# Optimization experiments

Measured on AMD Instinct MI355X. Metric: run time of the kernel, lower is better.

The kernel has to match this reference:

```python
import jax, jax.numpy as jnp
import numpy as np

T, B, D, H = 110, 256, 512, 512
EPS = 1e-9


def _forward(a, v, l, qmask, umask, mu_a, mu_v, mu_l, shifta, shiftv,
             turna, turnb, W1, b1, W2, b2):
    Tcur = a.shape[0]
    # ca = mu * (cos(a) + i sin(a)) = mu * exp(i a)
    ca = mu_a[:Tcur] * jnp.exp(1j * a)          # (T,B,D) complex64
    cv = mu_v[:Tcur] * jnp.exp(1j * v)
    cl = mu_l[:Tcur] * jnp.exp(1j * l)
    # phase shift of a and v streams, then sum into lav
    features = cl + ca * jnp.exp(1j * shifta) + cv * jnp.exp(1j * shiftv)  # (T,B,D)

    # --- step 0 (special-cased in the original loop) ---
    temp0 = features[0]                          # (B,D) complex
    qa0 = qmask[0][:, 0:1]                       # (B,1)
    qb0 = qmask[0][:, 1:2]
    ones = jnp.ones_like(temp0) * (1.0 + 1.0j)   # pA=pB=1+1j initial state
    pA0 = (1.0 - qa0) * ones + qa0 * temp0
    pB0 = (1.0 - qb0) * ones + qb0 * temp0

    # --- steps 1..T-1 as a fused scan over time ---
    def step(carry, xs):
        pA, pB = carry
        f, qm, ta, tb = xs                       # f:(B,D) cplx, qm:(B,2), ta/tb:(1,D)
        qa = qm[:, 0:1]
        qb = qm[:, 1:2]
        turn = qa * (pA * jnp.exp(1j * ta)) + qb * (pB * jnp.exp(1j * tb))
        # torch: turn.where(turn==0, turn/(abs+eps)) -> keep 0 where 0, else normalize
        turn = jnp.where(turn == 0, turn, turn / (jnp.abs(turn) + EPS))
        temp = f + turn
        pA = (1.0 - qa) * pA + qa * temp
        pB = (1.0 - qb) * pB + qb * temp
        return (pA, pB), temp

    (_, _), temps = jax.lax.scan(
        step, (pA0, pB0),
        (features[1:], qmask[1:], turna[1:Tcur], turnb[1:Tcur]))

    feats = jnp.concatenate([temp0[None], temps], axis=0)  # (T,B,D) complex
    fr, fi = feats.real, feats.imag
    f1r = fr @ W1.T + b1
    f1i = fi @ W1.T + b1
    f2r = fr @ W2.T + b2
    f2i = fi @ W2.T + b2
    xr = f1r - f2i
    xi = f1i + f2r
    return xr + xi                               # (T,B,H) float32


def setup_inputs() -> dict:
    key = jax.random.key(0)
    ks = jax.random.split(key, 12)
    a = jax.random.normal(ks[0], (T, B, D), jnp.float32)
    v = jax.random.normal(ks[1], (T, B, D), jnp.float32)
    l = jax.random.normal(ks[2], (T, B, D), jnp.float32)
    spk = jax.random.randint(ks[3], (T, B), 0, 2)
    qmask = jax.nn.one_hot(spk, 2, dtype=jnp.float32)      # (T,B,2)
    umask = jnp.ones((T, B), jnp.float32)                  # unused by forward
    mu_a = jnp.ones((110, 1, 1), jnp.float32)
    mu_v = jnp.ones((110, 1, 1), jnp.float32)
    mu_l = jnp.ones((110, 1, 1), jnp.float32)
    shifta = jax.random.normal(ks[4], (1, 1, D), jnp.float32)
    shiftv = jax.random.normal(ks[5], (1, 1, D), jnp.float32)
    turna = jax.random.uniform(ks[6], (110, 1, D), jnp.float32)
    turnb = jax.random.uniform(ks[7], (110, 1, D), jnp.float32)
    W1 = jax.random.normal(ks[8], (H, D), jnp.float32) * 0.02
    b1 = jnp.zeros((H,), jnp.float32)
    W2 = jax.random.normal(ks[9], (H, D), jnp.float32) * 0.02
    b2 = jnp.zeros((H,), jnp.float32)
    return {"a": a, "v": v, "l": l, "qmask": qmask, "umask": umask,
            "mu_a": mu_a, "mu_v": mu_v, "mu_l": mu_l,
            "shifta": shifta, "shiftv": shiftv,
            "turna": turna, "turnb": turnb,
            "W1": W1, "b1": b1, "W2": W2, "b2": b2,
            "dia_len": T}


def reference(a, v, l, qmask, umask, mu_a, mu_v, mu_l, shifta, shiftv,
              turna, turnb, W1, b1, W2, b2, dia_len):
    return _forward(a, v, l, qmask, umask, mu_a, mu_v, mu_l,
                    shifta, shiftv, turna, turnb, W1, b1, W2, b2)
```

## Files before the change

### kernel.cpp

```cpp
#include <hip/hip_runtime.h>

#define T_DIM 110
#define B_DIM 256
#define D_DIM 512
#define H_DIM 512
#define K_CAT 1024
#define M_DIM (T_DIM * B_DIM)
#define BD    (B_DIM * D_DIM)
#define EPSV 1e-9f

typedef float f32x4 __attribute__((ext_vector_type(4)));
typedef short bf16x8 __attribute__((ext_vector_type(8)));

static __device__ __forceinline__ unsigned short f2bf(float f) {
    unsigned u = __builtin_bit_cast(unsigned, f);
    u += 0x7fffu + ((u >> 16) & 1u);
    return (unsigned short)(u >> 16);
}

__global__ __launch_bounds__(256) void prep_w_kernel(
    const float* __restrict__ W1, const float* __restrict__ b1,
    const float* __restrict__ W2,
    unsigned short* __restrict__ Bt,
    float* __restrict__ bias2)
{
    int i = blockIdx.x * 256 + threadIdx.x;
    if (i < H_DIM) bias2[i] = 2.0f * b1[i];
    if (i >= H_DIM * K_CAT) return;
    int h = i / K_CAT;
    int k = i % K_CAT;
    float w;
    if (k < D_DIM) w = W1[h * D_DIM + k] + W2[h * D_DIM + k];
    else           w = W1[h * D_DIM + k - D_DIM] - W2[h * D_DIM + k - D_DIM];
    Bt[i] = f2bf(w);
}

__global__ __launch_bounds__(256) void feat_scan_kernel(
    const float* __restrict__ a, const float* __restrict__ v,
    const float* __restrict__ l, const float* __restrict__ qmask,
    const float* __restrict__ mu_a, const float* __restrict__ mu_v,
    const float* __restrict__ mu_l,
    const float* __restrict__ shifta, const float* __restrict__ shiftv,
    const float* __restrict__ turna, const float* __restrict__ turnb,
    unsigned short* __restrict__ A)
{
    const int tid = blockIdx.x * blockDim.x + threadIdx.x;
    const int b = tid >> 9;
    const int d = tid & 511;
    const float sa = shifta[d];
    const float sv = shiftv[d];

    float a0,v0,l0,ta0,tb0,q0,ma0,mv0,ml0;
    float a1,v1,l1,ta1,tb1,q1,ma1,mv1,ml1;
    float a2,v2,l2,ta2,tb2,q2,ma2,mv2,ml2;

#define LOAD_INTO(A_,V_,L_,TA_,TB_,Q_,MA_,MV_,ML_, T_)                        \
    {                                                                          \
        const int t_ = (T_);                                                   \
        A_  = a[(size_t)t_ * BD + tid];                                        \
        V_  = v[(size_t)t_ * BD + tid];                                        \
        L_  = l[(size_t)t_ * BD + tid];                                        \
        TA_ = turna[t_ * D_DIM + d];                                           \
        TB_ = turnb[t_ * D_DIM + d];                                           \
        Q_  = qmask[(size_t)(t_ * B_DIM + b) * 2];                             \
        MA_ = mu_a[t_]; MV_ = mu_v[t_]; ML_ = mu_l[t_];                        \
    }
#define PIN6(A_,V_,L_,TA_,TB_,Q_) \
    asm volatile("" : "+v"(A_), "+v"(V_), "+v"(L_), "+v"(TA_), "+v"(TB_), "+v"(Q_));

    LOAD_INTO(a0,v0,l0,ta0,tb0,q0,ma0,mv0,ml0, 0)
    LOAD_INTO(a1,v1,l1,ta1,tb1,q1,ma1,mv1,ml1, 1)
    LOAD_INTO(a2,v2,l2,ta2,tb2,q2,ma2,mv2,ml2, 2)
    PIN6(a0,v0,l0,ta0,tb0,q0)
    PIN6(a1,v1,l1,ta1,tb1,q1)
    PIN6(a2,v2,l2,ta2,tb2,q2)

    float pAr = 0.f, pAi = 0.f, pBr = 0.f, pBi = 0.f;

    #pragma unroll 3
    for (int t = 0; t < T_DIM; ++t) {
        float an,vn,ln,tan_,tbn,qn,man,mvn,mln;
        const int tp = (t + 3 < T_DIM) ? t + 3 : T_DIM - 1;
        LOAD_INTO(an,vn,ln,tan_,tbn,qn,man,mvn,mln, tp)
        PIN6(an,vn,ln,tan_,tbn,qn)

        float sA, cA, sV, cV, sL, cL;
        __sincosf(a0 + sa, &sA, &cA);
        __sincosf(v0 + sv, &sV, &cV);
        __sincosf(l0,      &sL, &cL);
        float fr = ml0 * cL + ma0 * cA + mv0 * cV;
        float fi = ml0 * sL + ma0 * sA + mv0 * sV;

        const bool isA = q0 > 0.5f;
        if (t == 0) {
            pAr = isA ? fr : 1.0f;  pAi = isA ? fi : 1.0f;
            pBr = isA ? 1.0f : fr;  pBi = isA ? 1.0f : fi;
        } else {
            float ph = isA ? ta0 : tb0;
            float pr = isA ? pAr : pBr;
            float pi = isA ? pAi : pBi;
            float sp, cp;
            __sincosf(ph, &sp, &cp);
            float tr = pr * cp - pi * sp;
            float ti = pr * sp + pi * cp;
            if (!(tr == 0.0f && ti == 0.0f)) {
                float inv = 1.0f / (sqrtf(tr * tr + ti * ti) + EPSV);
                tr *= inv; ti *= inv;
            }
            fr += tr;
            fi += ti;
            if (isA) { pAr = fr; pAi = fi; } else { pBr = fr; pBi = fi; }
        }

        const size_t row = (size_t)(t * B_DIM + b) * K_CAT;
        A[row + d]         = f2bf(fr);
        A[row + D_DIM + d] = f2bf(fi);

        a0=a1; v0=v1; l0=l1; ta0=ta1; tb0=tb1; q0=q1; ma0=ma1; mv0=mv1; ml0=ml1;
        a1=a2; v1=v2; l1=l2; ta1=ta2; tb1=tb2; q1=q2; ma1=ma2; mv1=mv2; ml1=ml2;
        a2=an; v2=vn; l2=ln; ta2=tan_; tb2=tbn; q2=qn; ma2=man; mv2=mvn; ml2=mln;
    }
#undef LOAD_INTO
#undef PIN6
}

#define BM 128
#define BN 128
#define BK 64

__global__ __launch_bounds__(256) void gemm_kernel(
    const unsigned short* __restrict__ A,
    const unsigned short* __restrict__ Bt,
    const float* __restrict__ bias2,
    float* __restrict__ C)
{
    __shared__ __align__(16) unsigned short As[BM * BK];
    __shared__ __align__(16) unsigned short Bs[BN * BK];

    const int tid = threadIdx.x;
    const int wave = tid >> 6;
    const int lane = tid & 63;
    const int wr = wave >> 1;
    const int wc = wave & 1;
    const int m0 = blockIdx.x * BM;
    const int n0 = blockIdx.y * BN;
    const int lrow = lane & 15;
    const int lk8 = (lane >> 4) * 8;

    const int srow = wave * 32;
    const int lrow8 = lane >> 3;
    const int lchunk = lane & 7;

    f32x4 acc[4][4] = {};

    for (int k0 = 0; k0 < K_CAT; k0 += BK) {
        #pragma unroll
        for (int c = 0; c < 4; ++c) {
            const int row = srow + c * 8 + lrow8;
            {
                const unsigned short* gp = A + (size_t)(m0 + row) * K_CAT + k0 + lchunk * 8;
                unsigned short* lp = As + (srow + c * 8) * BK + lane * 8;
                __builtin_amdgcn_global_load_lds(
                    (const __attribute__((address_space(1))) unsigned int*)gp,
                    (__attribute__((address_space(3))) unsigned int*)lp,
                    16, 0, 0);
            }
            {
                const unsigned short* gp = Bt + (size_t)(n0 + row) * K_CAT + k0 + lchunk * 8;
                unsigned short* lp = Bs + (srow + c * 8) * BK + lane * 8;
                __builtin_amdgcn_global_load_lds(
                    (const __attribute__((address_space(1))) unsigned int*)gp,
                    (__attribute__((address_space(3))) unsigned int*)lp,
                    16, 0, 0);
            }
        }
        __syncthreads();

        bf16x8 af[4][2], bfv[4][2];
        #pragma unroll
        for (int m = 0; m < 4; ++m)
            #pragma unroll
            for (int kk = 0; kk < 2; ++kk)
                af[m][kk] = *reinterpret_cast<const bf16x8*>(
                    &As[(wr * 64 + m * 16 + lrow) * BK + kk * 32 + lk8]);
        #pragma unroll
        for (int n = 0; n < 4; ++n)
            #pragma unroll
            for (int kk = 0; kk < 2; ++kk)
                bfv[n][kk] = *reinterpret_cast<const bf16x8*>(
                    &Bs[(wc * 64 + n * 16 + lrow) * BK + kk * 32 + lk8]);

        #pragma unroll
        for (int kk = 0; kk < 2; ++kk)
            #pragma unroll
            for (int m = 0; m < 4; ++m)
                #pragma unroll
                for (int n = 0; n < 4; ++n)
                    acc[m][n] = __builtin_amdgcn_mfma_f32_16x16x32_bf16(
                        af[m][kk], bfv[n][kk], acc[m][n], 0, 0, 0);
        __syncthreads();
    }

    const int rbase = m0 + wr * 64 + (lane >> 4) * 4;
    const int cbase = n0 + wc * 64;
    #pragma unroll
    for (int n = 0; n < 4; ++n) {
        const int col = cbase + n * 16 + lrow;
        const float bv = bias2[col];
        #pragma unroll
        for (int m = 0; m < 4; ++m) {
            const int row0 = rbase + m * 16;
            #pragma unroll
            for (int r = 0; r < 4; ++r) {
                C[(size_t)(row0 + r) * H_DIM + col] = acc[m][n][r] + bv;
            }
        }
    }
}

extern "C" void kernel_launch(void* const* d_in, const int* in_sizes, int n_in,
                              void* d_out, int out_size, void* d_ws, size_t ws_size,
                              hipStream_t stream) {
    const float* a      = (const float*)d_in[0];
    const float* v      = (const float*)d_in[1];
    const float* l      = (const float*)d_in[2];
    const float* qmask  = (const float*)d_in[3];
    const float* mu_a   = (const float*)d_in[5];
    const float* mu_v   = (const float*)d_in[6];
    const float* mu_l   = (const float*)d_in[7];
    const float* shifta = (const float*)d_in[8];
    const float* shiftv = (const float*)d_in[9];
    const float* turna  = (const float*)d_in[10];
    const float* turnb  = (const float*)d_in[11];
    const float* W1     = (const float*)d_in[12];
    const float* b1     = (const float*)d_in[13];
    const float* W2     = (const float*)d_in[14];
    float* out = (float*)d_out;

    char* ws = (char*)d_ws;
    unsigned short* Afeat = (unsigned short*)ws;
    size_t offB  = (size_t)M_DIM * K_CAT * sizeof(unsigned short);
    unsigned short* Bt = (unsigned short*)(ws + offB);
    size_t offBias = offB + (size_t)H_DIM * K_CAT * sizeof(unsigned short);
    float* bias2 = (float*)(ws + offBias);

    prep_w_kernel<<<(H_DIM * K_CAT + 255) / 256, 256, 0, stream>>>(W1, b1, W2, Bt, bias2);
    feat_scan_kernel<<<(B_DIM * D_DIM) / 256, 256, 0, stream>>>(
        a, v, l, qmask, mu_a, mu_v, mu_l, shifta, shiftv, turna, turnb, Afeat);
    dim3 grid(M_DIM / BM, H_DIM / BN);
    gemm_kernel<<<grid, 256, 0, stream>>>(Afeat, Bt, bias2, out);
}
```

Measured before the change: 136.4 us.

## Prefetch scan inputs through an LDS ring with direct global-to-LDS loads

The feature-scan kernel now streams each timestep's a, v, l, turna and turnb values straight from global memory into an 8-slot shared-memory ring using global_load_lds. It prefetches four steps ahead and gates each step with a manual s_waitcnt vmcnt. qmask and the mu scales are loaded once per block into shared memory instead of being fetched every step. The aim is to hide global load latency in the serial time loop without the register pressure of the old three-deep register rotation. The risk is that the hand-tuned vmcnt count, padded by duplicate prologue loads, silently depends on how the global stores to A are counted.

Result: slower. 161.8 us (+18.6%).

```diff
diff --git a/kernel.cpp b/kernel.cpp
--- a/kernel.cpp
+++ b/kernel.cpp
@@ -35,6 +35,9 @@
     Bt[i] = f2bf(w);
 }
 
+#define RING 8
+#define PFD  4
+
 __global__ __launch_bounds__(256) void feat_scan_kernel(
     const float* __restrict__ a, const float* __restrict__ v,
     const float* __restrict__ l, const float* __restrict__ qmask,
@@ -44,67 +47,90 @@
     const float* __restrict__ turna, const float* __restrict__ turnb,
     unsigned short* __restrict__ A)
 {
-    const int tid = blockIdx.x * blockDim.x + threadIdx.x;
-    const int b = tid >> 9;
-    const int d = tid & 511;
-    const float sa = shifta[d];
-    const float sv = shiftv[d];
-
-    float a0,v0,l0,ta0,tb0,q0,ma0,mv0,ml0;
-    float a1,v1,l1,ta1,tb1,q1,ma1,mv1,ml1;
-    float a2,v2,l2,ta2,tb2,q2,ma2,mv2,ml2;
-
-#define LOAD_INTO(A_,V_,L_,TA_,TB_,Q_,MA_,MV_,ML_, T_)                        \
+    __shared__ float ring[RING * 1280];
+    __shared__ float qm_s[T_DIM];
+    __shared__ float mu_s[3 * T_DIM];
+
+    const int tx = threadIdx.x;
+    const int b = blockIdx.x >> 1;
+    const int dbase = (blockIdx.x & 1) << 8;
+    const int d = dbase + tx;
+    const size_t gAVL = (size_t)b * D_DIM + d;
+
+    if (tx < T_DIM) {
+        qm_s[tx] = qmask[(size_t)(tx * B_DIM + b) * 2];
+        mu_s[tx]             = mu_a[tx];
+        mu_s[T_DIM + tx]     = mu_v[tx];
+        mu_s[2 * T_DIM + tx] = mu_l[tx];
+    }
+    const float sa = shifta[d & 511];
+    const float sv = shiftv[d & 511];
+    __syncthreads();
+
+#define GLL(gp, lp) __builtin_amdgcn_global_load_lds(                          \
+        (const __attribute__((address_space(1))) unsigned int*)(gp),           \
+        (__attribute__((address_space(3))) unsigned int*)(lp), 4, 0, 0)
+
+#define STAGE(tt, sl)                                                          \
     {                                                                          \
-        const int t_ = (T_);                                                   \
-        A_  = a[(size_t)t_ * BD + tid];                                        \
-        V_  = v[(size_t)t_ * BD + tid];                                        \
-        L_  = l[(size_t)t_ * BD + tid];                                        \
-        TA_ = turna[t_ * D_DIM + d];                                           \
-        TB_ = turnb[t_ * D_DIM + d];                                           \
-        Q_  = qmask[(size_t)(t_ * B_DIM + b) * 2];                             \
-        MA_ = mu_a[t_]; MV_ = mu_v[t_]; ML_ = mu_l[t_];                        \
-    }
-#define PIN6(A_,V_,L_,TA_,TB_,Q_) \
-    asm volatile("" : "+v"(A_), "+v"(V_), "+v"(L_), "+v"(TA_), "+v"(TB_), "+v"(Q_));
-
-    LOAD_INTO(a0,v0,l0,ta0,tb0,q0,ma0,mv0,ml0, 0)
-    LOAD_INTO(a1,v1,l1,ta1,tb1,q1,ma1,mv1,ml1, 1)
-    LOAD_INTO(a2,v2,l2,ta2,tb2,q2,ma2,mv2,ml2, 2)
-    PIN6(a0,v0,l0,ta0,tb0,q0)
-    PIN6(a1,v1,l1,ta1,tb1,q1)
-    PIN6(a2,v2,l2,ta2,tb2,q2)
+        const int t_ = (tt); const int s_ = (sl);                              \
+        GLL(a + (size_t)t_ * BD + gAVL,   &ring[s_ * 1280 +        tx]);       \
+        GLL(v + (size_t)t_ * BD + gAVL,   &ring[s_ * 1280 +  256 + tx]);       \
+        GLL(l + (size_t)t_ * BD + gAVL,   &ring[s_ * 1280 +  512 + tx]);       \
+        GLL(turna + t_ * D_DIM + d,       &ring[s_ * 1280 +  768 + tx]);       \
+        GLL(turnb + t_ * D_DIM + d,       &ring[s_ * 1280 + 1024 + tx]);       \
+    }
+#define SEP asm volatile("" ::: "memory")
+
+    STAGE(0, 0); SEP;
+    STAGE(1, 1); SEP;
+    STAGE(2, 2); SEP;
+    STAGE(3, 3); SEP;
+    STAGE(3, 3); SEP;
+    GLL(a + (size_t)3 * BD + gAVL, &ring[3 * 1280 +       tx]);
+    GLL(v + (size_t)3 * BD + gAVL, &ring[3 * 1280 + 256 + tx]);
+    GLL(l + (size_t)3 * BD + gAVL, &ring[3 * 1280 + 512 + tx]);
+    SEP;
 
     float pAr = 0.f, pAi = 0.f, pBr = 0.f, pBi = 0.f;
 
-    #pragma unroll 3
     for (int t = 0; t < T_DIM; ++t) {
-        float an,vn,ln,tan_,tbn,qn,man,mvn,mln;
-        const int tp = (t + 3 < T_DIM) ? t + 3 : T_DIM - 1;
-        LOAD_INTO(an,vn,ln,tan_,tbn,qn,man,mvn,mln, tp)
-        PIN6(an,vn,ln,tan_,tbn,qn)
+        const int tn = t + PFD;
+        STAGE(tn <= T_DIM - 1 ? tn : T_DIM - 1, tn & (RING - 1));
+        asm volatile("s_waitcnt vmcnt(24)" ::: "memory");
+
+        const int sl = t & (RING - 1);
+        const float av  = ring[sl * 1280 +        tx];
+        const float vv  = ring[sl * 1280 +  256 + tx];
+        const float lv  = ring[sl * 1280 +  512 + tx];
+        const float tav = ring[sl * 1280 +  768 + tx];
+        const float tbv = ring[sl * 1280 + 1024 + tx];
+        const float qa  = qm_s[t];
+        const float ma  = mu_s[t];
+        const float mv  = mu_s[T_DIM + t];
+        const float ml  = mu_s[2 * T_DIM + t];
 
         float sA, cA, sV, cV, sL, cL;
-        __sincosf(a0 + sa, &sA, &cA);
-        __sincosf(v0 + sv, &sV, &cV);
-        __sincosf(l0,      &sL, &cL);
-        float fr = ml0 * cL + ma0 * cA + mv0 * cV;
-        float fi = ml0 * sL + ma0 * sA + mv0 * sV;
-
-        const bool isA = q0 > 0.5f;
+        __sincosf(av + sa, &sA, &cA);
+        __sincosf(vv + sv, &sV, &cV);
+        __sincosf(lv,      &sL, &cL);
+        float fr = ml * cL + ma * cA + mv * cV;
+        float fi = ml * sL + ma * sA + mv * sV;
+
+        const bool isA = qa > 0.5f;
         if (t == 0) {
             pAr = isA ? fr : 1.0f;  pAi = isA ? fi : 1.0f;
             pBr = isA ? 1.0f : fr;  pBi = isA ? 1.0f : fi;
         } else {
-            float ph = isA ? ta0 : tb0;
-            float pr = isA ? pAr : pBr;
-            float pi = isA ? pAi : pBi;
+            const float ph = isA ? tav : tbv;
+            const float pr = isA ? pAr : pBr;
+            const float pi = isA ? pAi : pBi;
             float sp, cp;
             __sincosf(ph, &sp, &cp);
             float tr = pr * cp - pi * sp;
             float ti = pr * sp + pi * cp;
             if (!(tr == 0.0f && ti == 0.0f)) {
-                float inv = 1.0f / (sqrtf(tr * tr + ti * ti) + EPSV);
+                const float inv = 1.0f / (sqrtf(tr * tr + ti * ti) + EPSV);
                 tr *= inv; ti *= inv;
             }
             fr += tr;
@@ -115,13 +141,10 @@
         const size_t row = (size_t)(t * B_DIM + b) * K_CAT;
         A[row + d]         = f2bf(fr);
         A[row + D_DIM + d] = f2bf(fi);
-
-        a0=a1; v0=v1; l0=l1; ta0=ta1; tb0=tb1; q0=q1; ma0=ma1; mv0=mv1; ml0=ml1;
-        a1=a2; v1=v2; l1=l2; ta1=ta2; tb1=tb2; q1=q2; ma1=ma2; mv1=mv2; ml1=ml2;
-        a2=an; v2=vn; l2=ln; ta2=tan_; tb2=tbn; q2=qn; ma2=man; mv2=mvn; ml2=mln;
-    }
-#undef LOAD_INTO
-#undef PIN6
+    }
+#undef GLL
+#undef STAGE
+#undef SEP
 }
 
 #define BM 128
```

## Precompute turn phase sincos, interleave real/imag A columns, stage per-step scalars in LDS

Applied to the files above, without the earlier changes.

A new small kernel precomputes the cos/sin of turna and turnb into a float4 table, so the scan no longer evaluates sincos on the serial dependency chain. The feature matrix now stores the real and imaginary parts interleaved as one packed 32-bit write per element, and the weight prep permutes its K ordering to match. qmask and the mu values are staged in LDS per block, and the branchy zero check and t==0 special case are replaced with a multiplicative gate. The cost is an extra kernel launch and workspace for the table, and dropping the exact-zero check changes behaviour when turn is exactly zero.

New measurement: 113.5 us. 16.8% less time.

```diff
diff --git a/kernel.cpp b/kernel.cpp
--- a/kernel.cpp
+++ b/kernel.cpp
@@ -29,10 +29,22 @@
     if (i >= H_DIM * K_CAT) return;
     int h = i / K_CAT;
     int k = i % K_CAT;
-    float w;
-    if (k < D_DIM) w = W1[h * D_DIM + k] + W2[h * D_DIM + k];
-    else           w = W1[h * D_DIM + k - D_DIM] - W2[h * D_DIM + k - D_DIM];
+    int j = k >> 1;
+    float w = (k & 1) ? (W1[h * D_DIM + j] - W2[h * D_DIM + j])
+                      : (W1[h * D_DIM + j] + W2[h * D_DIM + j]);
     Bt[i] = f2bf(w);
+}
+
+__global__ __launch_bounds__(256) void prep_tt_kernel(
+    const float* __restrict__ turna, const float* __restrict__ turnb,
+    float4* __restrict__ TT)
+{
+    int i = blockIdx.x * 256 + threadIdx.x;
+    if (i >= T_DIM * D_DIM) return;
+    float s1, c1, s2, c2;
+    __sincosf(turna[i], &s1, &c1);
+    __sincosf(turnb[i], &s2, &c2);
+    TT[i] = make_float4(c1, s1, c2, s2);
 }
 
 __global__ __launch_bounds__(256) void feat_scan_kernel(
@@ -41,50 +53,50 @@
     const float* __restrict__ mu_a, const float* __restrict__ mu_v,
     const float* __restrict__ mu_l,
     const float* __restrict__ shifta, const float* __restrict__ shiftv,
-    const float* __restrict__ turna, const float* __restrict__ turnb,
-    unsigned short* __restrict__ A)
-{
-    const int tid = blockIdx.x * blockDim.x + threadIdx.x;
-    const int b = tid >> 9;
-    const int d = tid & 511;
+    const float4* __restrict__ TT,
+    unsigned int* __restrict__ A32)
+{
+    __shared__ float qm_s[T_DIM], mua_s[T_DIM], muv_s[T_DIM], mul_s[T_DIM];
+    const int tx = threadIdx.x;
+    const int b  = blockIdx.x >> 1;
+    const int d  = ((blockIdx.x & 1) << 8) + tx;
+    if (tx < T_DIM) {
+        qm_s[tx]  = qmask[(size_t)(tx * B_DIM + b) * 2];
+        mua_s[tx] = mu_a[tx];
+        muv_s[tx] = mu_v[tx];
+        mul_s[tx] = mu_l[tx];
+    }
     const float sa = shifta[d];
     const float sv = shiftv[d];
-
-    float a0,v0,l0,ta0,tb0,q0,ma0,mv0,ml0;
-    float a1,v1,l1,ta1,tb1,q1,ma1,mv1,ml1;
-    float a2,v2,l2,ta2,tb2,q2,ma2,mv2,ml2;
-
-#define LOAD_INTO(A_,V_,L_,TA_,TB_,Q_,MA_,MV_,ML_, T_)                        \
-    {                                                                          \
-        const int t_ = (T_);                                                   \
-        A_  = a[(size_t)t_ * BD + tid];                                        \
-        V_  = v[(size_t)t_ * BD + tid];                                        \
-        L_  = l[(size_t)t_ * BD + tid];                                        \
-        TA_ = turna[t_ * D_DIM + d];                                           \
-        TB_ = turnb[t_ * D_DIM + d];                                           \
-        Q_  = qmask[(size_t)(t_ * B_DIM + b) * 2];                             \
-        MA_ = mu_a[t_]; MV_ = mu_v[t_]; ML_ = mu_l[t_];                        \
-    }
-#define PIN6(A_,V_,L_,TA_,TB_,Q_) \
-    asm volatile("" : "+v"(A_), "+v"(V_), "+v"(L_), "+v"(TA_), "+v"(TB_), "+v"(Q_));
-
-    LOAD_INTO(a0,v0,l0,ta0,tb0,q0,ma0,mv0,ml0, 0)
-    LOAD_INTO(a1,v1,l1,ta1,tb1,q1,ma1,mv1,ml1, 1)
-    LOAD_INTO(a2,v2,l2,ta2,tb2,q2,ma2,mv2,ml2, 2)
-    PIN6(a0,v0,l0,ta0,tb0,q0)
-    PIN6(a1,v1,l1,ta1,tb1,q1)
-    PIN6(a2,v2,l2,ta2,tb2,q2)
-
-    float pAr = 0.f, pAi = 0.f, pBr = 0.f, pBi = 0.f;
+    __syncthreads();
+
+    const size_t gbase = (size_t)b * D_DIM + d;
+
+#define LDSET(A_,V_,L_,T4_,Q_,MA_,MV_,ML_, tt_)                                \
+    { const int t_ = (tt_);                                                    \
+      A_  = a[(size_t)t_ * BD + gbase];                                        \
+      V_  = v[(size_t)t_ * BD + gbase];                                        \
+      L_  = l[(size_t)t_ * BD + gbase];                                        \
+      T4_ = TT[t_ * D_DIM + d];                                                \
+      Q_  = qm_s[t_]; MA_ = mua_s[t_]; MV_ = muv_s[t_]; ML_ = mul_s[t_]; }
+
+    float a0,v0,l0,q0,ma0,mv0,ml0; float4 tt0;
+    float a1,v1,l1,q1,ma1,mv1,ml1; float4 tt1;
+    float a2,v2,l2,q2,ma2,mv2,ml2; float4 tt2;
+    LDSET(a0,v0,l0,tt0,q0,ma0,mv0,ml0, 0)
+    LDSET(a1,v1,l1,tt1,q1,ma1,mv1,ml1, 1)
+    LDSET(a2,v2,l2,tt2,q2,ma2,mv2,ml2, 2)
+
+    float pAr = 1.f, pAi = 1.f, pBr = 1.f, pBi = 1.f;
 
     #pragma unroll 3
     for (int t = 0; t < T_DIM; ++t) {
-        float an,vn,ln,tan_,tbn,qn,man,mvn,mln;
+        float aN,vN,lN,qN,maN,mvN,mlN; float4 ttN;
         const int tp = (t + 3 < T_DIM) ? t + 3 : T_DIM - 1;
-        LOAD_INTO(an,vn,ln,tan_,tbn,qn,man,mvn,mln, tp)
-        PIN6(an,vn,ln,tan_,tbn,qn)
-
-        float sA, cA, sV, cV, sL, cL;
+        LDSET(aN,vN,lN,ttN,qN,maN,mvN,mlN, tp)
+        __builtin_amdgcn_sched_barrier(0);
+
+        float sA,cA,sV,cV,sL,cL;
         __sincosf(a0 + sa, &sA, &cA);
         __sincosf(v0 + sv, &sV, &cV);
         __sincosf(l0,      &sL, &cL);
@@ -92,36 +104,27 @@
         float fi = ml0 * sL + ma0 * sA + mv0 * sV;
 
         const bool isA = q0 > 0.5f;
-        if (t == 0) {
-            pAr = isA ? fr : 1.0f;  pAi = isA ? fi : 1.0f;
-            pBr = isA ? 1.0f : fr;  pBi = isA ? 1.0f : fi;
-        } else {
-            float ph = isA ? ta0 : tb0;
-            float pr = isA ? pAr : pBr;
-            float pi = isA ? pAi : pBi;
-            float sp, cp;
-            __sincosf(ph, &sp, &cp);
-            float tr = pr * cp - pi * sp;
-            float ti = pr * sp + pi * cp;
-            if (!(tr == 0.0f && ti == 0.0f)) {
-                float inv = 1.0f / (sqrtf(tr * tr + ti * ti) + EPSV);
-                tr *= inv; ti *= inv;
-            }
-            fr += tr;
-            fi += ti;
-            if (isA) { pAr = fr; pAi = fi; } else { pBr = fr; pBi = fi; }
-        }
-
-        const size_t row = (size_t)(t * B_DIM + b) * K_CAT;
-        A[row + d]         = f2bf(fr);
-        A[row + D_DIM + d] = f2bf(fi);
-
-        a0=a1; v0=v1; l0=l1; ta0=ta1; tb0=tb1; q0=q1; ma0=ma1; mv0=mv1; ml0=ml1;
-        a1=a2; v1=v2; l1=l2; ta1=ta2; tb1=tb2; q1=q2; ma1=ma2; mv1=mv2; ml1=ml2;
-        a2=an; v2=vn; l2=ln; ta2=tan_; tb2=tbn; q2=qn; ma2=man; mv2=mvn; ml2=mln;
-    }
-#undef LOAD_INTO
-#undef PIN6
+        const float cp = isA ? tt0.x : tt0.z;
+        const float sp = isA ? tt0.y : tt0.w;
+        const float pr = isA ? pAr : pBr;
+        const float pi = isA ? pAi : pBi;
+        float tr = pr * cp - pi * sp;
+        float ti = pr * sp + pi * cp;
+        const float gate = (t == 0) ? 0.0f : 1.0f;
+        const float inv = gate / (sqrtf(tr * tr + ti * ti) + EPSV);
+        fr += tr * inv;
+        fi += ti * inv;
+        pAr = isA ? fr : pAr;  pAi = isA ? fi : pAi;
+        pBr = isA ? pBr : fr;  pBi = isA ? pBi : fi;
+
+        A32[(size_t)(t * B_DIM + b) * (K_CAT / 2) + d] =
+            (unsigned)f2bf(fr) | ((unsigned)f2bf(fi) << 16);
+
+        a0=a1; v0=v1; l0=l1; tt0=tt1; q0=q1; ma0=ma1; mv0=mv1; ml0=ml1;
+        a1=a2; v1=v2; l1=l2; tt1=tt2; q1=q2; ma1=ma2; mv1=mv2; ml1=ml2;
+        a2=aN; v2=vN; l2=lN; tt2=ttN; q2=qN; ma2=maN; mv2=mvN; ml2=mlN;
+    }
+#undef LDSET
 }
 
 #define BM 128
@@ -243,10 +246,13 @@
     unsigned short* Bt = (unsigned short*)(ws + offB);
     size_t offBias = offB + (size_t)H_DIM * K_CAT * sizeof(unsigned short);
     float* bias2 = (float*)(ws + offBias);
+    size_t offTT = offBias + 4096;
+    float4* TT = (float4*)(ws + offTT);
 
     prep_w_kernel<<<(H_DIM * K_CAT + 255) / 256, 256, 0, stream>>>(W1, b1, W2, Bt, bias2);
-    feat_scan_kernel<<<(B_DIM * D_DIM) / 256, 256, 0, stream>>>(
-        a, v, l, qmask, mu_a, mu_v, mu_l, shifta, shiftv, turna, turnb, Afeat);
+    prep_tt_kernel<<<(T_DIM * D_DIM + 255) / 256, 256, 0, stream>>>(turna, turnb, TT);
+    feat_scan_kernel<<<B_DIM * 2, 256, 0, stream>>>(
+        a, v, l, qmask, mu_a, mu_v, mu_l, shifta, shiftv, TT, (unsigned int*)Afeat);
     dim3 grid(M_DIM / BM, H_DIM / BN);
     gemm_kernel<<<grid, 256, 0, stream>>>(Afeat, Bt, bias2, out);
 }
```
